# Kernel tuning notes

Measured on AMD Instinct MI355X. Metric: run time of the kernel, lower is better.

The kernel has to match this reference:

```python
import jax, jax.numpy as jnp
import numpy as np

D = 1024
L_COMP = 16384
L_FULL = 32768
EPS = 1e-4


def setup_inputs() -> dict:
    key = jax.random.key(0)
    k1, k2 = jax.random.split(key)
    x = jax.random.normal(k1, (1, L_COMP, D), dtype=jnp.float32)
    p_selected = jax.random.uniform(k2, (L_COMP,), dtype=jnp.float32)
    # boundary mask over full sequence: exactly L_COMP ones, first position forced to 1
    rng = np.random.default_rng(0)
    pos = np.concatenate([[0], np.sort(rng.choice(np.arange(1, L_FULL), L_COMP - 1, replace=False))])
    b_np = np.zeros((1, L_FULL), dtype=np.int32)
    b_np[0, pos] = 1
    b = jnp.asarray(b_np)
    return {"x": x, "p_selected": p_selected, "b": b}


def _ema_scan(x, p):
    # z_t = (1 - p_t) * z_{t-1} + p_t * x_t  (exact math of the mamba chunk scan
    # with A=-1, dt=log(1/(1-p)), B=p, C=1, x pre-divided by dt)
    a = jnp.broadcast_to((1.0 - p)[None, :, None], x.shape)  # (1, L, d) decay
    bxt = p[None, :, None] * x                                # (1, L, d) input term

    def combine(c1, c2):
        a1, b1 = c1
        a2, b2 = c2
        return a1 * a2, a2 * b1 + b2

    _, z = jax.lax.associative_scan(combine, (a, bxt), axis=1)
    return z


def reference(x, p_selected, b):
    p = jnp.clip(p_selected.astype(jnp.float32), EPS, 1.0 - EPS)  # (L_comp,)
    z_bar = _ema_scan(x.astype(jnp.float32), p)                   # (1, L_comp, d)
    plug_back_idx = jnp.cumsum(b, axis=1) - 1                     # (1, L_full)
    out = jnp.take(z_bar[0], plug_back_idx[0], axis=0)[None]      # (1, L_full, d)
    return out.astype(x.dtype)
```

## Files before the change

kernel.cpp:

```cpp
#include <hip/hip_runtime.h>


#define DCH 1024
#define L_COMP 16384
#define L_FULL 32768
#define CHUNK 32
#define NCHUNK (L_COMP / CHUNK)
#define SEG (L_FULL / NCHUNK)
#define EPSV 1e-4f
#define WMIN 1e-12f

typedef float v4f __attribute__((ext_vector_type(4)));

__device__ __forceinline__ float clipp(float p) {
    p = fmaxf(p, EPSV);
    return fminf(p, 1.0f - EPSV);
}

__global__ __launch_bounds__(256, 2) void fused_kernel(
    const float* __restrict__ x, const float* __restrict__ p,
    const int* __restrict__ b, float* __restrict__ out) {
    const int c = blockIdx.x;
    const int tid = threadIdx.x;
    const int lane = tid & 63;
    const int wave = tid >> 6;
    const int base = c * CHUNK;

    __shared__ int bpref[NCHUNK + 1];
    __shared__ int spos[CHUNK + 1];
    __shared__ int wtot[4];

    {
        const int4* b4 = reinterpret_cast<const int4*>(b);
        int v0 = 0, v1 = 0;
#pragma unroll 4
        for (int q = 0; q < SEG / 4; ++q) {
            int4 w0 = b4[(2 * tid) * (SEG / 4) + q];
            int4 w1 = b4[(2 * tid + 1) * (SEG / 4) + q];
            v0 += w0.x + w0.y + w0.z + w0.w;
            v1 += w1.x + w1.y + w1.z + w1.w;
        }
        int s = v0 + v1;
        int incl = s;
#pragma unroll
        for (int off = 1; off < 64; off <<= 1) {
            int n = __shfl_up(incl, off, 64);
            if (lane >= off) incl += n;
        }
        if (lane == 63) wtot[wave] = incl;
        __syncthreads();
        int woff = 0;
        for (int w = 0; w < wave; ++w) woff += wtot[w];
        int ex = woff + incl - s;
        bpref[2 * tid] = ex;
        bpref[2 * tid + 1] = ex + v0;
        if (tid == 0) bpref[NCHUNK] = L_COMP;
        __syncthreads();
    }

    if (tid <= CHUNK) {
        int t = base + tid;
        int posv = L_FULL;
        if (t < L_COMP) {
            int lo = 0, hi = NCHUNK;
            while (hi - lo > 1) {
                int mid = (lo + hi) >> 1;
                if (bpref[mid] <= t) lo = mid; else hi = mid;
            }
            int lr = t - bpref[lo];
            const int4* bseg = reinterpret_cast<const int4*>(b) + lo * (SEG / 4);
            int cnt = 0;
#pragma unroll 4
            for (int q = 0; q < SEG / 4; ++q) {
                int4 w = bseg[q];
                if (w.x) { if (cnt == lr) posv = lo * SEG + 4 * q + 0; ++cnt; }
                if (w.y) { if (cnt == lr) posv = lo * SEG + 4 * q + 1; ++cnt; }
                if (w.z) { if (cnt == lr) posv = lo * SEG + 4 * q + 2; ++cnt; }
                if (w.w) { if (cnt == lr) posv = lo * SEG + 4 * q + 3; ++cnt; }
            }
        }
        spos[tid] = posv;
    }
    __syncthreads();

    int kstart = c;
    {
        float w = 1.0f;
        while (kstart > 0 && w >= WMIN) {
            --kstart;
            float ap = 1.0f;
#pragma unroll 8
            for (int t = 0; t < CHUNK; ++t)
                ap *= (1.0f - clipp(p[kstart * CHUNK + t]));
            w *= ap;
        }
    }

    {
        const v4f* x4 = reinterpret_cast<const v4f*>(x) + tid;
        v4f h = (v4f)0.f;
        for (int r = kstart * CHUNK; r < base; r += 8) {
            v4f xv[8];
            float pv[8];
#pragma unroll
            for (int j = 0; j < 8; ++j) {
                xv[j] = x4[(size_t)(r + j) * (DCH / 4)];
                pv[j] = clipp(p[r + j]);
            }
#pragma unroll
            for (int j = 0; j < 8; ++j) {
                float a = 1.0f - pv[j];
                h = a * h + pv[j] * xv[j];
            }
        }
        v4f* out4 = reinterpret_cast<v4f*>(out) + tid;
        int f0 = spos[0];
        for (int ib = 0; ib < CHUNK; ib += 8) {
            v4f xv[8];
            float pv[8];
            int fe[8];
#pragma unroll
            for (int j = 0; j < 8; ++j) {
                xv[j] = x4[(size_t)(base + ib + j) * (DCH / 4)];
                pv[j] = clipp(p[base + ib + j]);
                fe[j] = spos[ib + j + 1];
            }
#pragma unroll
            for (int j = 0; j < 8; ++j) {
                float a = 1.0f - pv[j];
                h = a * h + pv[j] * xv[j];
                for (int f = f0; f < fe[j]; ++f) {
                    __builtin_nontemporal_store(h, &out4[(size_t)f * (DCH / 4)]);
                }
                f0 = fe[j];
            }
        }
    }
}

extern "C" void kernel_launch(void* const* d_in, const int* in_sizes, int n_in,
                              void* d_out, int out_size, void* d_ws, size_t ws_size,
                              hipStream_t stream) {
    const float* x = (const float*)d_in[0];
    const float* p = (const float*)d_in[1];
    const int* b = (const int*)d_in[2];
    float* out = (float*)d_out;
    (void)d_ws; (void)ws_size;

    fused_kernel<<<NCHUNK, 256, 0, stream>>>(x, p, b, out);
}
```

Measured before the change: 204.2 us.

## Split fused scan into scan-to-workspace kernel plus gather broadcast kernel

Splits the fused kernel in two. The first kernel computes the EMA scan, writes z to a workspace buffer, and builds per-position gather indices with a prefix sum over b. The second kernel reads the indices and copies the matching z rows into the output with uniform, coalesced stores. This removes the binary search and per-segment position recovery, and the divergent variable-length store loops of the fused version. In exchange it adds a 64MB round trip through workspace, a second launch, and a fallback path for when the workspace is too small.

```diff
diff --git a/kernel.cpp b/kernel.cpp
--- a/kernel.cpp
+++ b/kernel.cpp
@@ -9,6 +9,10 @@
 #define SEG (L_FULL / NCHUNK)
 #define EPSV 1e-4f
 #define WMIN 1e-12f
+#define K2_ROWS 8
+#define WS_IDX_OFF 0
+#define WS_Z_OFF (128 * 1024)
+#define WS_NEED (WS_Z_OFF + (size_t)L_COMP * DCH * 4)
 
 typedef float v4f __attribute__((ext_vector_type(4)));
 
@@ -17,18 +21,66 @@
     return fminf(p, 1.0f - EPSV);
 }
 
-__global__ __launch_bounds__(256, 2) void fused_kernel(
+__global__ __launch_bounds__(256, 2) void scan_kernel(
     const float* __restrict__ x, const float* __restrict__ p,
-    const int* __restrict__ b, float* __restrict__ out) {
+    const int* __restrict__ b, float* __restrict__ z, int* __restrict__ idx) {
     const int c = blockIdx.x;
     const int tid = threadIdx.x;
     const int lane = tid & 63;
     const int wave = tid >> 6;
     const int base = c * CHUNK;
 
-    __shared__ int bpref[NCHUNK + 1];
-    __shared__ int spos[CHUNK + 1];
+    __shared__ int bpref[NCHUNK];
     __shared__ int wtot[4];
+
+    int kstart = c;
+    {
+        float w = 1.0f;
+        while (kstart > 0 && w >= WMIN) {
+            --kstart;
+            float ap = 1.0f;
+#pragma unroll 8
+            for (int t = 0; t < CHUNK; ++t)
+                ap *= (1.0f - clipp(p[kstart * CHUNK + t]));
+            w *= ap;
+        }
+    }
+
+    const v4f* x4 = reinterpret_cast<const v4f*>(x) + tid;
+    v4f h = (v4f)0.f;
+    for (int r = kstart * CHUNK; r < base; r += 8) {
+        v4f xw[8];
+        float pw[8];
+#pragma unroll
+        for (int j = 0; j < 8; ++j) {
+            xw[j] = x4[(size_t)(r + j) * (DCH / 4)];
+            pw[j] = clipp(p[r + j]);
+        }
+#pragma unroll
+        for (int j = 0; j < 8; ++j) {
+            float a = 1.0f - pw[j];
+            h = a * h + pw[j] * xw[j];
+        }
+    }
+
+    {
+        v4f* z4 = reinterpret_cast<v4f*>(z) + tid;
+        for (int ib = 0; ib < CHUNK; ib += 8) {
+            v4f xw[8];
+            float pw[8];
+#pragma unroll
+            for (int j = 0; j < 8; ++j) {
+                xw[j] = x4[(size_t)(base + ib + j) * (DCH / 4)];
+                pw[j] = clipp(p[base + ib + j]);
+            }
+#pragma unroll
+            for (int j = 0; j < 8; ++j) {
+                float a = 1.0f - pw[j];
+                h = a * h + pw[j] * xw[j];
+                z4[(size_t)(base + ib + j) * (DCH / 4)] = h;
+            }
+        }
+    }
 
     {
         const int4* b4 = reinterpret_cast<const int4*>(b);
@@ -54,10 +106,84 @@
         int ex = woff + incl - s;
         bpref[2 * tid] = ex;
         bpref[2 * tid + 1] = ex + v0;
+        __syncthreads();
+    }
+
+    if (wave == 0) {
+        int bv = b[c * SEG + lane];
+        int incl = bv;
+#pragma unroll
+        for (int off = 1; off < 64; off <<= 1) {
+            int n = __shfl_up(incl, off, 64);
+            if (lane >= off) incl += n;
+        }
+        idx[c * SEG + lane] = bpref[c] + incl - 1;
+    }
+}
+
+__global__ __launch_bounds__(256) void bcast_kernel(
+    const float* __restrict__ z, const int* __restrict__ idx,
+    float* __restrict__ out) {
+    const int tid = threadIdx.x;
+    const int r0 = blockIdx.x * K2_ROWS;
+
+    int zi[K2_ROWS];
+#pragma unroll
+    for (int j = 0; j < K2_ROWS; ++j)
+        zi[j] = idx[r0 + j];
+
+    const v4f* z4 = reinterpret_cast<const v4f*>(z) + tid;
+    v4f v[K2_ROWS];
+#pragma unroll
+    for (int j = 0; j < K2_ROWS; ++j)
+        v[j] = z4[(size_t)zi[j] * (DCH / 4)];
+
+    v4f* out4 = reinterpret_cast<v4f*>(out) + tid;
+#pragma unroll
+    for (int j = 0; j < K2_ROWS; ++j)
+        __builtin_nontemporal_store(v[j], &out4[(size_t)(r0 + j) * (DCH / 4)]);
+}
+
+__global__ __launch_bounds__(256, 2) void fused_fallback(
+    const float* __restrict__ x, const float* __restrict__ p,
+    const int* __restrict__ b, float* __restrict__ out) {
+    const int c = blockIdx.x;
+    const int tid = threadIdx.x;
+    const int lane = tid & 63;
+    const int wave = tid >> 6;
+    const int base = c * CHUNK;
+
+    __shared__ int bpref[NCHUNK + 1];
+    __shared__ int spos[CHUNK + 1];
+    __shared__ int wtot[4];
+
+    {
+        const int4* b4 = reinterpret_cast<const int4*>(b);
+        int v0 = 0, v1 = 0;
+#pragma unroll 4
+        for (int q = 0; q < SEG / 4; ++q) {
+            int4 w0 = b4[(2 * tid) * (SEG / 4) + q];
+            int4 w1 = b4[(2 * tid + 1) * (SEG / 4) + q];
+            v0 += w0.x + w0.y + w0.z + w0.w;
+            v1 += w1.x + w1.y + w1.z + w1.w;
+        }
+        int s = v0 + v1;
+        int incl = s;
+#pragma unroll
+        for (int off = 1; off < 64; off <<= 1) {
+            int n = __shfl_up(incl, off, 64);
+            if (lane >= off) incl += n;
+        }
+        if (lane == 63) wtot[wave] = incl;
+        __syncthreads();
+        int woff = 0;
+        for (int w = 0; w < wave; ++w) woff += wtot[w];
+        int ex = woff + incl - s;
+        bpref[2 * tid] = ex;
+        bpref[2 * tid + 1] = ex + v0;
         if (tid == 0) bpref[NCHUNK] = L_COMP;
         __syncthreads();
     }
-
     if (tid <= CHUNK) {
         int t = base + tid;
         int posv = L_FULL;
@@ -82,7 +208,6 @@
         spos[tid] = posv;
     }
     __syncthreads();
-
     int kstart = c;
     {
         float w = 1.0f;
@@ -95,7 +220,6 @@
             w *= ap;
         }
     }
-
     {
         const v4f* x4 = reinterpret_cast<const v4f*>(x) + tid;
         v4f h = (v4f)0.f;
@@ -129,9 +253,8 @@
             for (int j = 0; j < 8; ++j) {
                 float a = 1.0f - pv[j];
                 h = a * h + pv[j] * xv[j];
-                for (int f = f0; f < fe[j]; ++f) {
+                for (int f = f0; f < fe[j]; ++f)
                     __builtin_nontemporal_store(h, &out4[(size_t)f * (DCH / 4)]);
-                }
                 f0 = fe[j];
             }
         }
@@ -145,7 +268,14 @@
     const float* p = (const float*)d_in[1];
     const int* b = (const int*)d_in[2];
     float* out = (float*)d_out;
-    (void)d_ws; (void)ws_size;
-
-    fused_kernel<<<NCHUNK, 256, 0, stream>>>(x, p, b, out);
-}
+
+    if (ws_size >= WS_NEED) {
+        char* ws = (char*)d_ws;
+        int* idx = (int*)(ws + WS_IDX_OFF);
+        float* z = (float*)(ws + WS_Z_OFF);
+        scan_kernel<<<NCHUNK, 256, 0, stream>>>(x, p, b, z, idx);
+        bcast_kernel<<<L_FULL / K2_ROWS, 256, 0, stream>>>(z, idx, out);
+    } else {
+        fused_fallback<<<NCHUNK, 256, 0, stream>>>(x, p, b, out);
+    }
+}
```

Result: slower. 219.7 us (+7.6%).

## Split into index-prefix kernel and output-row-parallel scan kernel

Applied to the files above, without the earlier changes.

Adds a single-block kernel that computes the cumsum plug-back index for every output row into workspace. A second kernel then assigns each block 64 output rows, rebuilds the EMA state from a truncated warm-up window, and writes its rows. This removes the per-block redundant prefix sum and binary search over b in the fused kernel and balances work by output rows rather than input chunks. The cost is an extra launch plus a serial single-block index kernel, and the fused version is kept as a fallback when workspace is too small.

```diff
diff --git a/kernel.cpp b/kernel.cpp
--- a/kernel.cpp
+++ b/kernel.cpp
@@ -7,8 +7,11 @@
 #define CHUNK 32
 #define NCHUNK (L_COMP / CHUNK)
 #define SEG (L_FULL / NCHUNK)
+#define ROWS_PER_BLK 64
+#define NBLK (L_FULL / ROWS_PER_BLK)
 #define EPSV 1e-4f
 #define WMIN 1e-12f
+#define WS_NEED ((size_t)L_FULL * 4)
 
 typedef float v4f __attribute__((ext_vector_type(4)));
 
@@ -17,7 +20,127 @@
     return fminf(p, 1.0f - EPSV);
 }
 
-__global__ __launch_bounds__(256, 2) void fused_kernel(
+__global__ __launch_bounds__(1024) void idx_kernel(
+    const int* __restrict__ b, int* __restrict__ idx) {
+    const int tid = threadIdx.x;
+    const int lane = tid & 63;
+    const int wave = tid >> 6;
+    __shared__ int wtot[16];
+
+    int4 rb[8];
+    const int4* b4 = reinterpret_cast<const int4*>(b) + tid * 8;
+#pragma unroll
+    for (int q = 0; q < 8; ++q) rb[q] = b4[q];
+    int s = 0;
+#pragma unroll
+    for (int q = 0; q < 8; ++q) s += rb[q].x + rb[q].y + rb[q].z + rb[q].w;
+    int incl = s;
+#pragma unroll
+    for (int off = 1; off < 64; off <<= 1) {
+        int n = __shfl_up(incl, off, 64);
+        if (lane >= off) incl += n;
+    }
+    if (lane == 63) wtot[wave] = incl;
+    __syncthreads();
+    int woff = 0;
+    for (int w = 0; w < wave; ++w) woff += wtot[w];
+    int cum = woff + incl - s;
+    int* op = idx + tid * 32;
+#pragma unroll
+    for (int q = 0; q < 8; ++q) {
+        cum += rb[q].x; op[4 * q + 0] = cum - 1;
+        cum += rb[q].y; op[4 * q + 1] = cum - 1;
+        cum += rb[q].z; op[4 * q + 2] = cum - 1;
+        cum += rb[q].w; op[4 * q + 3] = cum - 1;
+    }
+}
+
+__global__ __launch_bounds__(256, 2) void bcast_scan_kernel(
+    const float* __restrict__ x, const float* __restrict__ p,
+    const int* __restrict__ idx, float* __restrict__ out) {
+    const int tid = threadIdx.x;
+    const int r0 = blockIdx.x * ROWS_PER_BLK;
+    __shared__ int sidx[ROWS_PER_BLK];
+
+    if (tid < ROWS_PER_BLK) sidx[tid] = idx[r0 + tid];
+    __syncthreads();
+    const int tmin = sidx[0];
+    const int tmax = sidx[ROWS_PER_BLK - 1];
+
+    int s0 = tmin;
+    {
+        float w = 1.0f;
+        while (s0 > 0 && w >= WMIN) {
+            if (s0 >= 16) {
+                float pw[16];
+#pragma unroll
+                for (int j = 0; j < 16; ++j) pw[j] = clipp(p[s0 - 16 + j]);
+#pragma unroll
+                for (int j = 0; j < 16; ++j) w *= (1.0f - pw[j]);
+                s0 -= 16;
+            } else {
+                for (int j = 0; j < s0; ++j) w *= (1.0f - clipp(p[j]));
+                s0 = 0;
+            }
+        }
+    }
+
+    const v4f* x4 = reinterpret_cast<const v4f*>(x) + tid;
+    v4f h = (v4f)0.f;
+    int r = s0;
+    for (; r + 8 <= tmin; r += 8) {
+        v4f xw[8];
+        float pw[8];
+#pragma unroll
+        for (int j = 0; j < 8; ++j) {
+            xw[j] = x4[(size_t)(r + j) * (DCH / 4)];
+            pw[j] = clipp(p[r + j]);
+        }
+#pragma unroll
+        for (int j = 0; j < 8; ++j) {
+            float a = 1.0f - pw[j];
+            h = a * h + pw[j] * xw[j];
+        }
+    }
+    for (; r < tmin; ++r) {
+        v4f xw = x4[(size_t)r * (DCH / 4)];
+        float pw = clipp(p[r]);
+        h = (1.0f - pw) * h + pw * xw;
+    }
+
+    v4f* out4 = reinterpret_cast<v4f*>(out) + tid;
+    int j = 0;
+    int t = tmin;
+    for (; t + 8 <= tmax + 1; t += 8) {
+        v4f xw[8];
+        float pw[8];
+#pragma unroll
+        for (int q = 0; q < 8; ++q) {
+            xw[q] = x4[(size_t)(t + q) * (DCH / 4)];
+            pw[q] = clipp(p[t + q]);
+        }
+#pragma unroll
+        for (int q = 0; q < 8; ++q) {
+            float a = 1.0f - pw[q];
+            h = a * h + pw[q] * xw[q];
+            while (j < ROWS_PER_BLK && sidx[j] == t + q) {
+                __builtin_nontemporal_store(h, &out4[(size_t)(r0 + j) * (DCH / 4)]);
+                ++j;
+            }
+        }
+    }
+    for (; t <= tmax; ++t) {
+        v4f xw = x4[(size_t)t * (DCH / 4)];
+        float pw = clipp(p[t]);
+        h = (1.0f - pw) * h + pw * xw;
+        while (j < ROWS_PER_BLK && sidx[j] == t) {
+            __builtin_nontemporal_store(h, &out4[(size_t)(r0 + j) * (DCH / 4)]);
+            ++j;
+        }
+    }
+}
+
+__global__ __launch_bounds__(256, 2) void fused_fallback(
     const float* __restrict__ x, const float* __restrict__ p,
     const int* __restrict__ b, float* __restrict__ out) {
     const int c = blockIdx.x;
@@ -57,7 +180,6 @@
         if (tid == 0) bpref[NCHUNK] = L_COMP;
         __syncthreads();
     }
-
     if (tid <= CHUNK) {
         int t = base + tid;
         int posv = L_FULL;
@@ -82,7 +204,6 @@
         spos[tid] = posv;
     }
     __syncthreads();
-
     int kstart = c;
     {
         float w = 1.0f;
@@ -95,7 +216,6 @@
             w *= ap;
         }
     }
-
     {
         const v4f* x4 = reinterpret_cast<const v4f*>(x) + tid;
         v4f h = (v4f)0.f;
@@ -129,9 +249,8 @@
             for (int j = 0; j < 8; ++j) {
                 float a = 1.0f - pv[j];
                 h = a * h + pv[j] * xv[j];
-                for (int f = f0; f < fe[j]; ++f) {
+                for (int f = f0; f < fe[j]; ++f)
                     __builtin_nontemporal_store(h, &out4[(size_t)f * (DCH / 4)]);
-                }
                 f0 = fe[j];
             }
         }
@@ -145,7 +264,12 @@
     const float* p = (const float*)d_in[1];
     const int* b = (const int*)d_in[2];
     float* out = (float*)d_out;
-    (void)d_ws; (void)ws_size;
-
-    fused_kernel<<<NCHUNK, 256, 0, stream>>>(x, p, b, out);
-}
+
+    if (ws_size >= WS_NEED) {
+        int* idx = (int*)d_ws;
+        idx_kernel<<<1, 1024, 0, stream>>>(b, idx);
+        bcast_scan_kernel<<<NBLK, 256, 0, stream>>>(x, p, idx, out);
+    } else {
+        fused_fallback<<<NCHUNK, 256, 0, stream>>>(x, p, b, out);
+    }
+}
```

Measured after the change: 205.6 us. About the same (+0.7%).
